# Kernel tuning notes

Measured on AMD Instinct MI355X. Metric: run time of the kernel, lower is better.

## Reference

```python
import jax, jax.numpy as jnp
import numpy as np

B, S, K, N = 4, 2048, 4096, 4096


def setup_inputs() -> dict:
    key = jax.random.key(0)
    k1, k2, k3, k4 = jax.random.split(key, 4)
    x = jax.random.normal(k1, (B, S, K), dtype=jnp.float32)
    # int8 quantized weight values in [-128, 127], stored as int32 (jax-friendly container)
    qw = jax.random.randint(k2, (N, K), -128, 128, dtype=jnp.int32)
    # per-tensor scale: amax/127 style scalar
    sw = (jax.random.uniform(k3, (), dtype=jnp.float32) * 0.02 + 0.001)
    bias = jax.random.normal(k4, (N,), dtype=jnp.float32)
    return {"x": x, "qw": qw, "sw": sw, "bias": bias}


def reference(x, qw, sw, bias):
    # per_tensor_matmul: dequantize weight to fp32 with scalar scale, fp32 GEMM, cast back, add bias
    x_dtype = x.dtype
    w = qw.astype(jnp.float32) * sw          # [N, K] dequantized
    y = jnp.einsum('bsk,nk->bsn', x.astype(jnp.float32), w).astype(x_dtype)
    y = y + bias                              # [B, S, N]
    return y
```

## Files before the change

kernel.cpp:

```cpp
#include <hip/hip_runtime.h>
#include <stdint.h>

#define MDIM 8192
#define NDIM 4096
#define KDIM 4096

#define BM 256
#define BN 256
#define BK 128
#define NKT (KDIM / BK)

typedef __attribute__((ext_vector_type(4)))  int i32x4;
typedef __attribute__((ext_vector_type(16))) int i32x16;

#define AS1 __attribute__((address_space(1)))
#define AS3 __attribute__((address_space(3)))

__device__ __forceinline__ int clamp127(int v) {
    return v > 127 ? 127 : (v < -127 ? -127 : v);
}

__global__ __launch_bounds__(256) void quant_x(
        const float* __restrict__ x, const float* __restrict__ sw,
        int8_t* __restrict__ Aq, float* __restrict__ scales) {
    const int row = blockIdx.x;
    const int t   = threadIdx.x;
    const float4* px = (const float4*)(x + (size_t)row * KDIM);

    float4 v[4];
#pragma unroll
    for (int j = 0; j < 4; j++) v[j] = px[t + 256 * j];

    float a = 0.f;
#pragma unroll
    for (int j = 0; j < 4; j++) {
        a = fmaxf(a, fabsf(v[j].x)); a = fmaxf(a, fabsf(v[j].y));
        a = fmaxf(a, fabsf(v[j].z)); a = fmaxf(a, fabsf(v[j].w));
    }
#pragma unroll
    for (int off = 32; off >= 1; off >>= 1)
        a = fmaxf(a, __shfl_xor(a, off));
    __shared__ float red[4];
    if ((t & 63) == 0) red[t >> 6] = a;
    __syncthreads();
    const float amax = fmaxf(fmaxf(red[0], red[1]), fmaxf(red[2], red[3]));
    const float inv  = (amax > 0.f) ? (127.0f / amax) : 0.f;
    if (t == 0) scales[row] = (amax * (1.0f / 127.0f)) * (*sw);

    int* out32 = (int*)(Aq + (size_t)row * KDIM);
#pragma unroll
    for (int j = 0; j < 4; j++) {
        int b0 = clamp127(__float2int_rn(v[j].x * inv));
        int b1 = clamp127(__float2int_rn(v[j].y * inv));
        int b2 = clamp127(__float2int_rn(v[j].z * inv));
        int b3 = clamp127(__float2int_rn(v[j].w * inv));
        out32[t + 256 * j] = (b0 & 255) | ((b1 & 255) << 8) | ((b2 & 255) << 16) | ((b3 & 255) << 24);
    }
}

__global__ __launch_bounds__(256) void cvt_w(const int* __restrict__ qw, int8_t* __restrict__ Bq) {
    const long i = (long)blockIdx.x * 256 + threadIdx.x;
    int4 a = ((const int4*)qw)[i];
    ((int*)Bq)[i] = (a.x & 255) | ((a.y & 255) << 8) | ((a.z & 255) << 16) | ((a.w & 255) << 24);
}


#define BAR()    do { asm volatile("" ::: "memory"); __builtin_amdgcn_s_barrier(); asm volatile("" ::: "memory"); } while (0)
#define WAITV(n) asm volatile("s_waitcnt vmcnt(" #n ")" ::: "memory")

#define STAGE_A(buf, h, kt) do { \
    __builtin_amdgcn_global_load_lds((AS1 const void*)(gA + (size_t)((h) * 128) * KDIM + (kt) * 128), \
        (AS3 void*)(sA + (buf) * 32768 + (h) * 16384 + sdst), 16, 0, 0); \
    __builtin_amdgcn_global_load_lds((AS1 const void*)(gA + (size_t)((h) * 128 + 64) * KDIM + (kt) * 128), \
        (AS3 void*)(sA + (buf) * 32768 + (h) * 16384 + 8192 + sdst), 16, 0, 0); \
} while (0)

#define STAGE_B(buf, h, kt) do { \
    __builtin_amdgcn_global_load_lds((AS1 const void*)(gB + (size_t)((h) * 128) * KDIM + (kt) * 128), \
        (AS3 void*)(sB + (buf) * 32768 + (h) * 16384 + sdst), 16, 0, 0); \
    __builtin_amdgcn_global_load_lds((AS1 const void*)(gB + (size_t)((h) * 128 + 64) * KDIM + (kt) * 128), \
        (AS3 void*)(sB + (buf) * 32768 + (h) * 16384 + 8192 + sdst), 16, 0, 0); \
} while (0)

#define READ_A0(buf) do { \
    _Pragma("unroll") for (int q = 0; q < 2; ++q) \
    _Pragma("unroll") for (int ks = 0; ks < 4; ++ks) \
        aF0[q][ks] = *(const i32x4*)(sA + (buf) * 32768 + rbA + q * 4096 + co[ks]); \
} while (0)

#define READ_A1(buf) do { \
    _Pragma("unroll") for (int q = 0; q < 2; ++q) \
    _Pragma("unroll") for (int ks = 0; ks < 4; ++ks) \
        aF1[q][ks] = *(const i32x4*)(sA + (buf) * 32768 + rbA + (2 + q) * 4096 + co[ks]); \
} while (0)

#define READ_Bb(buf) do { \
    _Pragma("unroll") for (int ni = 0; ni < 2; ++ni) \
    _Pragma("unroll") for (int ks = 0; ks < 4; ++ks) \
        bF[ni][ks] = *(const i32x4*)(sB + (buf) * 32768 + rbB + (ni) * 4096 + co[ks]); \
} while (0)

#define MMA0(ni) do { \
    __builtin_amdgcn_s_setprio(1); \
    _Pragma("unroll") for (int ks = 0; ks < 4; ++ks) { \
        acc[0][ni] = __builtin_amdgcn_mfma_i32_32x32x32_i8(aF0[0][ks], bF[ni][ks], acc[0][ni], 0, 0, 0); \
        acc[1][ni] = __builtin_amdgcn_mfma_i32_32x32x32_i8(aF0[1][ks], bF[ni][ks], acc[1][ni], 0, 0, 0); \
    } \
    __builtin_amdgcn_s_setprio(0); \
} while (0)

#define MMA1(ni) do { \
    __builtin_amdgcn_s_setprio(1); \
    _Pragma("unroll") for (int ks = 0; ks < 4; ++ks) { \
        acc[2][ni] = __builtin_amdgcn_mfma_i32_32x32x32_i8(aF1[0][ks], bF[ni][ks], acc[2][ni], 0, 0, 0); \
        acc[3][ni] = __builtin_amdgcn_mfma_i32_32x32x32_i8(aF1[1][ks], bF[ni][ks], acc[3][ni], 0, 0, 0); \
    } \
    __builtin_amdgcn_s_setprio(0); \
} while (0)

__global__ __launch_bounds__(512, 2) void gemm_bt_i8(
        const int8_t* __restrict__ A,
        const int8_t* __restrict__ Bm,
        const float* __restrict__ scales,
        const float* __restrict__ bias,
        float* __restrict__ C)
{
    __shared__ __align__(16) int8_t sA[2 * BM * BK];
    __shared__ __align__(16) int8_t sB[2 * BN * BK];

    const int tid  = threadIdx.x;
    const int wave = tid >> 6;
    const int lane = tid & 63;
    const int wr   = wave >> 2;
    const int wc   = wave & 3;
    const int l32  = lane & 31;
    const int hi   = lane >> 5;

    const int orig = blockIdx.y * 16 + blockIdx.x;
    const int nu   = (orig & 7) * 64 + (orig >> 3);
    const int m0   = (nu >> 4) * BM;
    const int n0   = (nu & 15) * BN;

    const int trow = tid >> 3;
    const int slog = (tid & 7) ^ (trow & 7);
    const int8_t* gA = A  + (size_t)(m0 + trow) * KDIM + slog * 16;
    const int8_t* gB = Bm + (size_t)(n0 + trow) * KDIM + slog * 16;
    const int sdst = tid * 16;

    const int swz = l32 & 7;
    const int rbA = (wr * 128 + l32) * BK;
    const int rbB = (wc * 64  + l32) * BK;
    int co[4];
#pragma unroll
    for (int ks = 0; ks < 4; ++ks) co[ks] = ((((ks << 1) | hi) ^ swz) << 4);

    i32x16 acc[4][2];
#pragma unroll
    for (int mi = 0; mi < 4; ++mi)
#pragma unroll
        for (int ni = 0; ni < 2; ++ni)
#pragma unroll
            for (int r = 0; r < 16; ++r) acc[mi][ni][r] = 0;

    i32x4 aF0[2][4];
    i32x4 aF1[2][4];
    i32x4 bF[2][4];

    STAGE_B(0, 0, 0); STAGE_B(0, 1, 0);
    STAGE_A(0, 0, 0); STAGE_A(0, 1, 0);
    STAGE_B(1, 0, 1); STAGE_B(1, 1, 1);
    STAGE_A(1, 0, 1); STAGE_A(1, 1, 1);
    WAITV(8);
    BAR();

#pragma unroll 1
    for (int it = 0; it < NKT / 2 - 1; ++it) {
        const int t2 = 2 * it + 2, t3 = 2 * it + 3;
        READ_A0(0); READ_Bb(0);                    BAR(); MMA0(0); BAR();
        READ_A1(0);                                BAR(); MMA0(1); BAR();
        STAGE_B(0, 0, t2);                         BAR(); MMA1(1); BAR();
        STAGE_B(0, 1, t2); WAITV(4);               BAR(); MMA1(0); BAR();
        READ_A0(1); READ_Bb(1);
        STAGE_A(0, 0, t2); STAGE_A(0, 1, t2);      BAR(); MMA0(0); BAR();
        READ_A1(1);                                BAR(); MMA0(1); BAR();
        STAGE_B(1, 0, t3); STAGE_B(1, 1, t3);      BAR(); MMA1(1); BAR();
        STAGE_A(1, 0, t3); STAGE_A(1, 1, t3); WAITV(8); BAR(); MMA1(0); BAR();
    }

    READ_A0(0); READ_Bb(0);                        BAR(); MMA0(0); BAR();
    READ_A1(0);                                    BAR(); MMA0(1); BAR();
                                                   BAR(); MMA1(1); BAR();
    WAITV(0);                                      BAR(); MMA1(0); BAR();
    READ_A0(1); READ_Bb(1);                        BAR(); MMA0(0); BAR();
    READ_A1(1);                                    BAR(); MMA0(1); BAR();
    MMA1(1);
    MMA1(0);

#pragma unroll
    for (int mi = 0; mi < 4; ++mi) {
        const int row_base = m0 + wr * 128 + mi * 32 + 4 * hi;
        float sc[16];
#pragma unroll
        for (int r = 0; r < 16; ++r)
            sc[r] = scales[row_base + (r & 3) + 8 * (r >> 2)];
#pragma unroll
        for (int ni = 0; ni < 2; ++ni) {
            const int col = n0 + wc * 64 + ni * 32 + l32;
            const float bc = bias[col];
#pragma unroll
            for (int r = 0; r < 16; ++r) {
                const int row = row_base + (r & 3) + 8 * (r >> 2);
                C[(size_t)row * NDIM + col] = (float)acc[mi][ni][r] * sc[r] + bc;
            }
        }
    }
}

__global__ void gemm_naive_f32(const float* __restrict__ x, const int* __restrict__ qw,
                               const float* __restrict__ sw, const float* __restrict__ bias,
                               float* __restrict__ out) {
    size_t id = (size_t)blockIdx.x * blockDim.x + threadIdx.x;
    if (id >= (size_t)MDIM * NDIM) return;
    int m = (int)(id / NDIM);
    int n = (int)(id % NDIM);
    const float* xr = x + (size_t)m * KDIM;
    const int*   wr = qw + (size_t)n * KDIM;
    float acc = 0.f;
    for (int k = 0; k < KDIM; k++) acc += xr[k] * (float)wr[k];
    out[id] = acc * (*sw) + bias[n];
}

extern "C" void kernel_launch(void* const* d_in, const int* in_sizes, int n_in,
                              void* d_out, int out_size, void* d_ws, size_t ws_size,
                              hipStream_t stream) {
    const float* x    = (const float*)d_in[0];
    const int*   qw   = (const int*)d_in[1];
    const float* sw   = (const float*)d_in[2];
    const float* bias = (const float*)d_in[3];
    float* out = (float*)d_out;

    const size_t needA = (size_t)MDIM * KDIM;
    const size_t needB = (size_t)NDIM * KDIM;
    const size_t needS = (size_t)MDIM * sizeof(float);

    if (ws_size >= needA + needB + needS) {
        int8_t* Aq = (int8_t*)d_ws;
        int8_t* Bq = Aq + needA;
        float*  scales = (float*)(Bq + needB);

        quant_x<<<MDIM, 256, 0, stream>>>(x, sw, Aq, scales);
        const long nw4 = (long)NDIM * KDIM / 4;
        cvt_w<<<(int)(nw4 / 256), 256, 0, stream>>>(qw, Bq);

        dim3 grid(NDIM / BN, MDIM / BM);
        gemm_bt_i8<<<grid, 512, 0, stream>>>(Aq, Bq, scales, bias, out);
    } else {
        size_t total = (size_t)MDIM * NDIM;
        gemm_naive_f32<<<(total + 255) / 256, 256, 0, stream>>>(x, qw, sw, bias, out);
    }
}
```

Measured before the change: 406.7 us.

## Switch int8 GEMM to 16x16x64 MFMA tiles with matching LDS swizzle

Replaces the 32x32x32 int8 MFMA with the 16x16x64 int8 variant. The per-wave 128x64 tile becomes 8x4 accumulators of 16x16, and the LDS read offsets and staging swizzle are rewritten to fit the new fragment layout. The epilogue is remapped to the 16x16 output layout. The goal is a different MFMA issue pattern and less LDS bank conflict, at the cost of more MFMA instructions and a different register and fragment layout that could carry layout bugs.

```diff
diff --git a/kernel.cpp b/kernel.cpp
--- a/kernel.cpp
+++ b/kernel.cpp
@@ -11,7 +11,6 @@
 #define NKT (KDIM / BK)
 
 typedef __attribute__((ext_vector_type(4)))  int i32x4;
-typedef __attribute__((ext_vector_type(16))) int i32x16;
 
 #define AS1 __attribute__((address_space(1)))
 #define AS3 __attribute__((address_space(3)))
@@ -83,38 +82,40 @@
 } while (0)
 
 #define READ_A0(buf) do { \
-    _Pragma("unroll") for (int q = 0; q < 2; ++q) \
-    _Pragma("unroll") for (int ks = 0; ks < 4; ++ks) \
-        aF0[q][ks] = *(const i32x4*)(sA + (buf) * 32768 + rbA + q * 4096 + co[ks]); \
+    _Pragma("unroll") for (int mi = 0; mi < 4; ++mi) \
+    _Pragma("unroll") for (int ks = 0; ks < 2; ++ks) \
+        aF0[mi][ks] = *(const i32x4*)(sA + (buf) * 32768 + rbA + mi * 2048 + co[ks]); \
 } while (0)
 
 #define READ_A1(buf) do { \
-    _Pragma("unroll") for (int q = 0; q < 2; ++q) \
-    _Pragma("unroll") for (int ks = 0; ks < 4; ++ks) \
-        aF1[q][ks] = *(const i32x4*)(sA + (buf) * 32768 + rbA + (2 + q) * 4096 + co[ks]); \
+    _Pragma("unroll") for (int mi = 0; mi < 4; ++mi) \
+    _Pragma("unroll") for (int ks = 0; ks < 2; ++ks) \
+        aF1[mi][ks] = *(const i32x4*)(sA + (buf) * 32768 + rbA + (4 + mi) * 2048 + co[ks]); \
 } while (0)
 
 #define READ_Bb(buf) do { \
-    _Pragma("unroll") for (int ni = 0; ni < 2; ++ni) \
-    _Pragma("unroll") for (int ks = 0; ks < 4; ++ks) \
-        bF[ni][ks] = *(const i32x4*)(sB + (buf) * 32768 + rbB + (ni) * 4096 + co[ks]); \
-} while (0)
-
-#define MMA0(ni) do { \
+    _Pragma("unroll") for (int ni = 0; ni < 4; ++ni) \
+    _Pragma("unroll") for (int ks = 0; ks < 2; ++ks) \
+        bF[ni][ks] = *(const i32x4*)(sB + (buf) * 32768 + rbB + ni * 2048 + co[ks]); \
+} while (0)
+
+#define MMA0(nh) do { \
     __builtin_amdgcn_s_setprio(1); \
-    _Pragma("unroll") for (int ks = 0; ks < 4; ++ks) { \
-        acc[0][ni] = __builtin_amdgcn_mfma_i32_32x32x32_i8(aF0[0][ks], bF[ni][ks], acc[0][ni], 0, 0, 0); \
-        acc[1][ni] = __builtin_amdgcn_mfma_i32_32x32x32_i8(aF0[1][ks], bF[ni][ks], acc[1][ni], 0, 0, 0); \
-    } \
+    _Pragma("unroll") for (int ks = 0; ks < 2; ++ks) \
+    _Pragma("unroll") for (int mi = 0; mi < 4; ++mi) \
+    _Pragma("unroll") for (int nj = 0; nj < 2; ++nj) \
+        acc[mi][2 * (nh) + nj] = __builtin_amdgcn_mfma_i32_16x16x64_i8( \
+            aF0[mi][ks], bF[2 * (nh) + nj][ks], acc[mi][2 * (nh) + nj], 0, 0, 0); \
     __builtin_amdgcn_s_setprio(0); \
 } while (0)
 
-#define MMA1(ni) do { \
+#define MMA1(nh) do { \
     __builtin_amdgcn_s_setprio(1); \
-    _Pragma("unroll") for (int ks = 0; ks < 4; ++ks) { \
-        acc[2][ni] = __builtin_amdgcn_mfma_i32_32x32x32_i8(aF1[0][ks], bF[ni][ks], acc[2][ni], 0, 0, 0); \
-        acc[3][ni] = __builtin_amdgcn_mfma_i32_32x32x32_i8(aF1[1][ks], bF[ni][ks], acc[3][ni], 0, 0, 0); \
-    } \
+    _Pragma("unroll") for (int ks = 0; ks < 2; ++ks) \
+    _Pragma("unroll") for (int mi = 0; mi < 4; ++mi) \
+    _Pragma("unroll") for (int nj = 0; nj < 2; ++nj) \
+        acc[4 + mi][2 * (nh) + nj] = __builtin_amdgcn_mfma_i32_16x16x64_i8( \
+            aF1[mi][ks], bF[2 * (nh) + nj][ks], acc[4 + mi][2 * (nh) + nj], 0, 0, 0); \
     __builtin_amdgcn_s_setprio(0); \
 } while (0)
 
@@ -133,8 +134,8 @@
     const int lane = tid & 63;
     const int wr   = wave >> 2;
     const int wc   = wave & 3;
-    const int l32  = lane & 31;
-    const int hi   = lane >> 5;
+    const int lr   = lane & 15;
+    const int lg   = lane >> 4;
 
     const int orig = blockIdx.y * 16 + blockIdx.x;
     const int nu   = (orig & 7) * 64 + (orig >> 3);
@@ -142,29 +143,29 @@
     const int n0   = (nu & 15) * BN;
 
     const int trow = tid >> 3;
-    const int slog = (tid & 7) ^ (trow & 7);
+    const int slog = (tid & 7) ^ (((tid >> 5) & 1) << 1);
     const int8_t* gA = A  + (size_t)(m0 + trow) * KDIM + slog * 16;
     const int8_t* gB = Bm + (size_t)(n0 + trow) * KDIM + slog * 16;
     const int sdst = tid * 16;
 
-    const int swz = l32 & 7;
-    const int rbA = (wr * 128 + l32) * BK;
-    const int rbB = (wc * 64  + l32) * BK;
-    int co[4];
-#pragma unroll
-    for (int ks = 0; ks < 4; ++ks) co[ks] = ((((ks << 1) | hi) ^ swz) << 4);
-
-    i32x16 acc[4][2];
-#pragma unroll
-    for (int mi = 0; mi < 4; ++mi)
-#pragma unroll
-        for (int ni = 0; ni < 2; ++ni)
-#pragma unroll
-            for (int r = 0; r < 16; ++r) acc[mi][ni][r] = 0;
-
-    i32x4 aF0[2][4];
-    i32x4 aF1[2][4];
-    i32x4 bF[2][4];
+    const int f = ((lr >> 2) & 1) << 1;
+    const int rbA = (wr * 128 + lr) * BK;
+    const int rbB = (wc * 64  + lr) * BK;
+    int co[2];
+#pragma unroll
+    for (int ks = 0; ks < 2; ++ks) co[ks] = ks * 64 + ((lg ^ f) << 4);
+
+    i32x4 acc[8][4];
+#pragma unroll
+    for (int mi = 0; mi < 8; ++mi)
+#pragma unroll
+        for (int ni = 0; ni < 4; ++ni)
+#pragma unroll
+            for (int r = 0; r < 4; ++r) acc[mi][ni][r] = 0;
+
+    i32x4 aF0[4][2];
+    i32x4 aF1[4][2];
+    i32x4 bF[4][2];
 
     STAGE_B(0, 0, 0); STAGE_B(0, 1, 0);
     STAGE_A(0, 0, 0); STAGE_A(0, 1, 0);
@@ -197,21 +198,18 @@
     MMA1(0);
 
 #pragma unroll
-    for (int mi = 0; mi < 4; ++mi) {
-        const int row_base = m0 + wr * 128 + mi * 32 + 4 * hi;
-        float sc[16];
-#pragma unroll
-        for (int r = 0; r < 16; ++r)
-            sc[r] = scales[row_base + (r & 3) + 8 * (r >> 2)];
-#pragma unroll
-        for (int ni = 0; ni < 2; ++ni) {
-            const int col = n0 + wc * 64 + ni * 32 + l32;
+    for (int mi = 0; mi < 8; ++mi) {
+        const int row_base = m0 + wr * 128 + mi * 16 + lg * 4;
+        float sc[4];
+#pragma unroll
+        for (int r = 0; r < 4; ++r) sc[r] = scales[row_base + r];
+#pragma unroll
+        for (int ni = 0; ni < 4; ++ni) {
+            const int col = n0 + wc * 64 + ni * 16 + lr;
             const float bc = bias[col];
 #pragma unroll
-            for (int r = 0; r < 16; ++r) {
-                const int row = row_base + (r & 3) + 8 * (r >> 2);
-                C[(size_t)row * NDIM + col] = (float)acc[mi][ni][r] * sc[r] + bc;
-            }
+            for (int r = 0; r < 4; ++r)
+                C[(size_t)(row_base + r) * NDIM + col] = (float)acc[mi][ni][r] * sc[r] + bc;
         }
     }
 }
```

Result: no change. 405.7 us (-0.3%).
